# Kernel optimization log

Measured on AMD Instinct MI355X. Metric: run time of the kernel, lower is better.

## Reference

```python
import jax, jax.numpy as jnp
import numpy as np

B, S, D = 8, 2048, 768
H = 4 * D  # MLP hidden
EPS = 1e-5


def setup_inputs() -> dict:
    key = jax.random.key(0)
    ks = jax.random.split(key, 12)
    sd = 1.0 / np.sqrt(D)
    sh = 1.0 / np.sqrt(H)
    return {
        "x": jax.random.normal(ks[0], (B, S, D), dtype=jnp.float32),
        "ln1_g": jnp.ones((D,), jnp.float32),
        "ln1_b": jnp.zeros((D,), jnp.float32),
        "ln2_g": jnp.ones((D,), jnp.float32),
        "ln2_b": jnp.zeros((D,), jnp.float32),
        "Wq": jax.random.normal(ks[1], (D, D), jnp.float32) * sd,
        "bq": jnp.zeros((D,), jnp.float32),
        "Wk": jax.random.normal(ks[2], (D, D), jnp.float32) * sd,
        "bk": jnp.zeros((D,), jnp.float32),
        "Wv": jax.random.normal(ks[3], (D, D), jnp.float32) * sd,
        "bv": jnp.zeros((D,), jnp.float32),
        "Wo": jax.random.normal(ks[4], (D, D), jnp.float32) * sd,
        "bo": jnp.zeros((D,), jnp.float32),
        "Wfc": jax.random.normal(ks[5], (D, H), jnp.float32) * sd,
        "bfc": jnp.zeros((H,), jnp.float32),
        "Wproj": jax.random.normal(ks[6], (H, D), jnp.float32) * sh,
        "bproj": jnp.zeros((D,), jnp.float32),
    }


def _layernorm(x, g, b):
    mu = jnp.mean(x, axis=-1, keepdims=True)
    var = jnp.mean(jnp.square(x - mu), axis=-1, keepdims=True)
    return (x - mu) * jax.lax.rsqrt(var + EPS) * g + b


def reference(x, ln1_g, ln1_b, ln2_g, ln2_b, Wq, bq, Wk, bk, Wv, bv, Wo, bo,
              Wfc, bfc, Wproj, bproj):
    d = x.shape[-1]
    # --- attention sub-block (single head, full D) ---
    h = _layernorm(x, ln1_g, ln1_b)
    q = h @ Wq + bq            # [B,S,D]
    k = h @ Wk + bk
    v = h @ Wv + bv
    scores = jnp.einsum("bsd,btd->bst", q, k) / jnp.sqrt(jnp.float32(d))
    attn = jax.nn.softmax(scores, axis=-1)  # softmax over keys (dim=2)
    y = jnp.einsum("bst,btd->bsd", attn, v)
    x = x + (y @ Wo + bo)
    # --- MLP sub-block (exact GELU like nn.GELU default) ---
    h2 = _layernorm(x, ln2_g, ln2_b)
    m = jax.nn.gelu(h2 @ Wfc + bfc, approximate=False)
    x = x + (m @ Wproj + bproj)  # dropout p=0 -> identity
    return x
```

## Files before the change

kernel.cpp:

```cpp
#include <hip/hip_runtime.h>
#include <hip/hip_bf16.h>

typedef __attribute__((ext_vector_type(8))) short short8;
typedef __attribute__((ext_vector_type(4))) float floatx4;

using bf16 = __hip_bfloat16;

__device__ __forceinline__ void cp16_g2l(bf16* lds_p, const bf16* g) {
  __builtin_amdgcn_global_load_lds(
      (const __attribute__((address_space(1))) unsigned int*)g,
      (__attribute__((address_space(3))) unsigned int*)lds_p,
      16, 0, 0);
}

__device__ __forceinline__ float gelu_exact(float x) {
  return 0.5f * x * (1.0f + erff(x * 0.70710678118654752f));
}

template<int MODE>
__global__ __launch_bounds__(256)
void gemm_bt(const bf16* __restrict__ A, long sAb, long lda,
             const bf16* __restrict__ Bt, long sBb, long ldb,
             const float* __restrict__ bias,
             const float* __restrict__ resid,
             float* __restrict__ rsum, long rsS, long cbStr,
             void* __restrict__ out, long sOb,
             int N, int K, float scale)
{
  constexpr bool PA = (MODE == 5);

  __shared__ __attribute__((aligned(16))) bf16 sA[2][128 * 32];
  __shared__ __attribute__((aligned(16))) bf16 sB[2][128 * 32];

  const int tid = threadIdx.x;
  const int l = tid & 63, w = tid >> 6;
  const int bz = blockIdx.z;
  const long row0 = (long)blockIdx.x * 128;
  const long col0 = (long)blockIdx.y * 128;

  const bf16* Ab = A + (long)bz * sAb;
  const bf16* Bb = Bt + (long)bz * sBb;

  const int sr = (w << 4) + (l >> 2);
  const int slot = (l & 3) ^ ((sr >> 1) & 3);
  const int kcd = (l & 3) << 3;
  const bf16* gA;
  long skipA, koA;
  if constexpr (PA) {
    gA    = Ab + ((long)(slot >> 1) * lda + row0 + sr) * 16 + ((slot & 1) << 3);
    skipA = 64 * 16;
    koA   = 32 * lda;
  } else {
    gA    = Ab + (row0 + sr) * lda + (slot << 3);
    skipA = 64 * lda;
    koA   = 32;
  }
  const bf16* gB = Bb + (col0 + sr) * ldb + (slot << 3);
  const long skipB = 64 * ldb;
  bf16* lA = &sA[0][sr * 32 + kcd];
  bf16* lB = &sB[0][sr * 32 + kcd];

  floatx4 acc[4][4];
  #pragma unroll
  for (int i = 0; i < 4; ++i)
    #pragma unroll
    for (int j = 0; j < 4; ++j)
      acc[i][j] = (floatx4){0.f, 0.f, 0.f, 0.f};

  const int wr = (w >> 1) & 1, wc = w & 1;
  const int g = l >> 4, t = l & 15;
  const int swz = (g ^ ((t >> 1) & 3)) << 3;
  const int aoff = (wr * 64 + t) * 32 + swz;
  const int boff = (wc * 64 + t) * 32 + swz;

  const int nt = K >> 5;

  cp16_g2l(lA,           gA);
  cp16_g2l(lA + 64 * 32, gA + skipA);
  cp16_g2l(lB,           gB);
  cp16_g2l(lB + 64 * 32, gB + skipB);
  __syncthreads();

  for (int kt = 0; kt < nt; ++kt) {
    const int cur = kt & 1;
    if (kt + 1 < nt) {
      const long oA = (long)(kt + 1) * koA;
      const long oB = (long)(kt + 1) << 5;
      bf16* dA = lA + (cur ^ 1) * (128 * 32);
      bf16* dB = lB + (cur ^ 1) * (128 * 32);
      cp16_g2l(dA,           gA + oA);
      cp16_g2l(dA + 64 * 32, gA + oA + skipA);
      cp16_g2l(dB,           gB + oB);
      cp16_g2l(dB + 64 * 32, gB + oB + skipB);
    }
    const bf16* cA = &sA[cur][0];
    const bf16* cB = &sB[cur][0];
    short8 a[4], b[4];
    #pragma unroll
    for (int m = 0; m < 4; ++m) a[m] = *(const short8*)(cA + aoff + m * 512);
    #pragma unroll
    for (int n = 0; n < 4; ++n) b[n] = *(const short8*)(cB + boff + n * 512);
    #pragma unroll
    for (int m = 0; m < 4; ++m)
      #pragma unroll
      for (int n = 0; n < 4; ++n)
        acc[m][n] = __builtin_amdgcn_mfma_f32_16x16x32_bf16(a[m], b[n], acc[m][n], 0, 0, 0);
    __syncthreads();
  }

  const long orow = row0 + wr * 64 + (g << 2);
  const long ocol = col0 + wc * 64 + t;

  if constexpr (MODE == 0 || MODE == 4) {
    bf16* O = (bf16*)out + (long)bz * sOb;
    float bv4[4];
    #pragma unroll
    for (int n = 0; n < 4; ++n) bv4[n] = bias[ocol + n * 16];
    #pragma unroll
    for (int m = 0; m < 4; ++m) {
      #pragma unroll
      for (int r = 0; r < 4; ++r) {
        bf16* Or = O + (orow + m * 16 + r) * (long)N + ocol;
        #pragma unroll
        for (int n = 0; n < 4; ++n) {
          float vv = acc[m][n][r] + bv4[n];
          if constexpr (MODE == 4) vv = gelu_exact(vv);
          Or[n * 16] = __float2bfloat16(vv);
        }
      }
    }
  } else if constexpr (MODE == 3) {
    float* O = (float*)out;
    float bv4[4];
    #pragma unroll
    for (int n = 0; n < 4; ++n) bv4[n] = bias[ocol + n * 16];
    #pragma unroll
    for (int m = 0; m < 4; ++m) {
      #pragma unroll
      for (int r = 0; r < 4; ++r) {
        const long rb = (orow + m * 16 + r) * (long)N + ocol;
        #pragma unroll
        for (int n = 0; n < 4; ++n)
          O[rb + n * 16] = acc[m][n][r] + bv4[n] + resid[rb + n * 16];
      }
    }
  } else if constexpr (MODE == 5) {
    bf16* O = (bf16*)out + (long)bz * sOb;
    #pragma unroll
    for (int m = 0; m < 4; ++m) {
      #pragma unroll
      for (int r = 0; r < 4; ++r) {
        const long rr = orow + m * 16 + r;
        const float inv = 1.0f / rsum[bz * rsS + rr];
        bf16* Or = O + rr * (long)N + ocol;
        #pragma unroll
        for (int n = 0; n < 4; ++n)
          Or[n * 16] = __float2bfloat16(acc[m][n][r] * inv);
      }
    }
  } else {
    bf16* O = (bf16*)out + (long)bz * sOb;
    const long pb = (col0 >> 4) + wc * 4;
    float prow[4][4];
    #pragma unroll
    for (int m = 0; m < 4; ++m)
      #pragma unroll
      for (int r = 0; r < 4; ++r) prow[m][r] = 0.f;
    #pragma unroll
    for (int n = 0; n < 4; ++n) {
      bf16* Opan = O + (pb + n) * (rsS * 16) + t;
      #pragma unroll
      for (int m = 0; m < 4; ++m) {
        #pragma unroll
        for (int r = 0; r < 4; ++r) {
          const float p = __expf(acc[m][n][r] * scale);
          Opan[(orow + m * 16 + r) * 16] = __float2bfloat16(p);
          prow[m][r] += p;
        }
      }
    }
    #pragma unroll
    for (int m = 0; m < 4; ++m) {
      #pragma unroll
      for (int r = 0; r < 4; ++r) {
        float s = prow[m][r];
        s += __shfl_xor(s, 1);
        s += __shfl_xor(s, 2);
        s += __shfl_xor(s, 4);
        s += __shfl_xor(s, 8);
        if (t == 0)
          rsum[(long)(blockIdx.y * 2 + wc) * cbStr + bz * rsS +
               orow + m * 16 + r] = s;
      }
    }
  }
}

__global__ __launch_bounds__(256)
void reduce32(const float* __restrict__ rp, float* __restrict__ rs, int n)
{
  const int i = threadIdx.x + blockIdx.x * 256;
  if (i < n) {
    float s = 0.f;
    #pragma unroll
    for (int c = 0; c < 32; ++c) s += rp[(long)c * 16384 + i];
    rs[i] = s;
  }
}

__global__ __launch_bounds__(256)
void ln_kernel(const float* __restrict__ X, const float* __restrict__ G,
               const float* __restrict__ Bv, bf16* __restrict__ H)
{
  const int tid = threadIdx.x;
  const long row = blockIdx.x;
  const float* xr = X + row * 768;
  const float v0 = xr[tid], v1 = xr[tid + 256], v2 = xr[tid + 512];
  float s = v0 + v1 + v2;
  float s2 = v0 * v0 + v1 * v1 + v2 * v2;
  #pragma unroll
  for (int o = 32; o > 0; o >>= 1) {
    s += __shfl_xor(s, o);
    s2 += __shfl_xor(s2, o);
  }
  __shared__ float red[8];
  const int w = tid >> 6, l = tid & 63;
  if (l == 0) { red[w] = s; red[w + 4] = s2; }
  __syncthreads();
  s = red[0] + red[1] + red[2] + red[3];
  s2 = red[4] + red[5] + red[6] + red[7];
  const float mu = s * (1.f / 768.f);
  const float var = s2 * (1.f / 768.f) - mu * mu;
  const float rstd = rsqrtf(var + 1e-5f);
  bf16* hr = H + row * 768;
  hr[tid]       = __float2bfloat16((v0 - mu) * rstd * G[tid]       + Bv[tid]);
  hr[tid + 256] = __float2bfloat16((v1 - mu) * rstd * G[tid + 256] + Bv[tid + 256]);
  hr[tid + 512] = __float2bfloat16((v2 - mu) * rstd * G[tid + 512] + Bv[tid + 512]);
}

__global__ void transpose_w(const float* __restrict__ W, bf16* __restrict__ Wt,
                            int K, int N)
{
  __shared__ float tile[32][33];
  const int n0 = blockIdx.x * 32, k0 = blockIdx.y * 32;
  const int tx = threadIdx.x, ty = threadIdx.y;
  #pragma unroll
  for (int j = ty; j < 32; j += 8)
    tile[j][tx] = W[(long)(k0 + j) * N + n0 + tx];
  __syncthreads();
  #pragma unroll
  for (int j = ty; j < 32; j += 8)
    Wt[(long)(n0 + j) * K + k0 + tx] = __float2bfloat16(tile[tx][j]);
}

__global__ void transpose_v(const bf16* __restrict__ QKV, bf16* __restrict__ Vt)
{
  __shared__ bf16 tile[32][33];
  const int d0 = blockIdx.x * 32, s0 = blockIdx.y * 32, b = blockIdx.z;
  const int tx = threadIdx.x, ty = threadIdx.y;
  #pragma unroll
  for (int j = ty; j < 32; j += 8)
    tile[j][tx] = QKV[((long)b * 2048 + s0 + j) * 2304 + 1536 + d0 + tx];
  __syncthreads();
  #pragma unroll
  for (int j = ty; j < 32; j += 8)
    Vt[(long)b * 768 * 2048 + (long)(d0 + j) * 2048 + s0 + tx] = tile[tx][j];
}

__global__ void concat3(const float* __restrict__ a, const float* __restrict__ b,
                        const float* __restrict__ c, float* __restrict__ o)
{
  const int i = threadIdx.x + blockIdx.x * 256;
  if (i < 768) { o[i] = a[i]; o[i + 768] = b[i]; o[i + 1536] = c[i]; }
}

extern "C" void kernel_launch(void* const* d_in, const int* in_sizes, int n_in,
                              void* d_out, int out_size, void* d_ws, size_t ws_size,
                              hipStream_t stream)
{
  const float* x     = (const float*)d_in[0];
  const float* ln1g  = (const float*)d_in[1];
  const float* ln1b  = (const float*)d_in[2];
  const float* ln2g  = (const float*)d_in[3];
  const float* ln2b  = (const float*)d_in[4];
  const float* Wq    = (const float*)d_in[5];
  const float* bq    = (const float*)d_in[6];
  const float* Wk    = (const float*)d_in[7];
  const float* bk    = (const float*)d_in[8];
  const float* Wv    = (const float*)d_in[9];
  const float* bvv   = (const float*)d_in[10];
  const float* Wo    = (const float*)d_in[11];
  const float* bo    = (const float*)d_in[12];
  const float* Wfc   = (const float*)d_in[13];
  const float* bfc   = (const float*)d_in[14];
  const float* Wproj = (const float*)d_in[15];
  const float* bproj = (const float*)d_in[16];
  float* out = (float*)d_out;

  constexpr int Bz = 8, S = 2048, D = 768, Hh = 3072, QKVN = 3 * D;
  constexpr long Mtot = (long)Bz * S;

  char* ws = (char*)d_ws;
  size_t off = 0;
  auto alloc = [&](size_t bytes) -> char* {
    char* p = ws + off;
    off += (bytes + 255) & ~(size_t)255;
    return p;
  };
  bf16* wqkvT = (bf16*)alloc((size_t)QKVN * D * 2);
  bf16* woT   = (bf16*)alloc((size_t)D * D * 2);
  bf16* wfcT  = (bf16*)alloc((size_t)Hh * D * 2);
  bf16* wprT  = (bf16*)alloc((size_t)D * Hh * 2);
  float* bqkv = (float*)alloc((size_t)QKVN * 4);
  float* rsum = (float*)alloc((size_t)Mtot * 4);
  float* rpart= (float*)alloc((size_t)32 * Mtot * 4);
  bf16* hb    = (bf16*)alloc((size_t)Mtot * D * 2);
  bf16* qkv   = (bf16*)alloc((size_t)Mtot * QKVN * 2);
  bf16* vtb   = (bf16*)alloc((size_t)Mtot * D * 2);
  bf16* yb    = (bf16*)alloc((size_t)Mtot * D * 2);

  int nbat = Bz;
  size_t region = (size_t)nbat * S * S * 2;
  const size_t mbytes = (size_t)Mtot * Hh * 2;
  if (region < mbytes) region = mbytes;
  if (off + region > ws_size) {
    nbat = 1;
    region = mbytes;
  }
  char* reg = alloc(region);
  bf16* attn = (bf16*)reg;
  bf16* mb = (bf16*)reg;

  const dim3 tb(32, 8);

  transpose_w<<<dim3(D / 32, D / 32), tb, 0, stream>>>(Wq, wqkvT, D, D);
  transpose_w<<<dim3(D / 32, D / 32), tb, 0, stream>>>(Wk, wqkvT + (size_t)D * D, D, D);
  transpose_w<<<dim3(D / 32, D / 32), tb, 0, stream>>>(Wv, wqkvT + 2 * (size_t)D * D, D, D);
  transpose_w<<<dim3(D / 32, D / 32), tb, 0, stream>>>(Wo, woT, D, D);
  transpose_w<<<dim3(Hh / 32, D / 32), tb, 0, stream>>>(Wfc, wfcT, D, Hh);
  transpose_w<<<dim3(D / 32, Hh / 32), tb, 0, stream>>>(Wproj, wprT, Hh, D);
  concat3<<<3, 256, 0, stream>>>(bq, bk, bvv, bqkv);

  ln_kernel<<<(int)Mtot, 256, 0, stream>>>(x, ln1g, ln1b, hb);

  gemm_bt<0><<<dim3(Mtot / 128, QKVN / 128, 1), 256, 0, stream>>>(
      hb, 0, D, wqkvT, 0, D, bqkv, nullptr, nullptr, 0, 0, qkv, 0, QKVN, D, 1.f);
  transpose_v<<<dim3(D / 32, S / 32, Bz), tb, 0, stream>>>(qkv, vtb);

  const float sc = 0.03608439182435161f;
  for (int g0 = 0; g0 < Bz; g0 += nbat) {
    const bf16* qg  = qkv + (long)g0 * S * QKVN;
    const bf16* kg  = qkv + (long)g0 * S * QKVN + D;
    const bf16* vtg = vtb + (long)g0 * D * S;
    float* rsg = rsum + (long)g0 * S;
    float* rpg = rpart + (long)g0 * S;
    bf16* yg = yb + (long)g0 * S * D;
    gemm_bt<6><<<dim3(S / 128, S / 128, nbat), 256, 0, stream>>>(
        qg, (long)S * QKVN, QKVN, kg, (long)S * QKVN, QKVN, nullptr, nullptr,
        rpg, S, Mtot, attn, (long)S * S, S, D, sc);
    reduce32<<<(int)(Mtot / 256), 256, 0, stream>>>(rpart, rsum, (int)Mtot);
    gemm_bt<5><<<dim3(S / 128, D / 128, nbat), 256, 0, stream>>>(
        attn, (long)S * S, S, vtg, (long)D * S, S, nullptr, nullptr,
        rsg, S, 0, yg, (long)S * D, D, S, 1.f);
  }

  gemm_bt<3><<<dim3(Mtot / 128, D / 128, 1), 256, 0, stream>>>(
      yb, 0, D, woT, 0, D, bo, x, nullptr, 0, 0, out, 0, D, D, 1.f);

  ln_kernel<<<(int)Mtot, 256, 0, stream>>>(out, ln2g, ln2b, hb);

  gemm_bt<4><<<dim3(Mtot / 128, Hh / 128, 1), 256, 0, stream>>>(
      hb, 0, D, wfcT, 0, D, bfc, nullptr, nullptr, 0, 0, mb, 0, Hh, D, 1.f);
  gemm_bt<3><<<dim3(Mtot / 128, D / 128, 1), 256, 0, stream>>>(
      mb, 0, Hh, wprT, 0, Hh, bproj, out, nullptr, 0, 0, out, 0, D, Hh, 1.f);
}
```

Measured before the change: 665.0 us.

## Use triple-buffered LDS with one barrier per k-step and partial vmcnt waits

Moves the GEMM main loop from two LDS buffers to three, issues the next tile's global-to-LDS loads, then waits only for the older loads (vmcnt(4)) before a single raw s_barrier. The trailing __syncthreads is removed, because the third buffer keeps the slot being overwritten from matching any slot still being read. The goal is to cut barrier count and let loads overlap MFMA work. In exchange LDS use grows from 32KB to 48KB per block, which may reduce occupancy, and correctness now depends on hand-written waitcnt values.

```diff
diff --git a/kernel.cpp b/kernel.cpp
--- a/kernel.cpp
+++ b/kernel.cpp
@@ -29,8 +29,8 @@
 {
   constexpr bool PA = (MODE == 5);
 
-  __shared__ __attribute__((aligned(16))) bf16 sA[2][128 * 32];
-  __shared__ __attribute__((aligned(16))) bf16 sB[2][128 * 32];
+  __shared__ __attribute__((aligned(16))) bf16 sA[3][128 * 32];
+  __shared__ __attribute__((aligned(16))) bf16 sB[3][128 * 32];
 
   const int tid = threadIdx.x;
   const int l = tid & 63, w = tid >> 6;
@@ -57,8 +57,7 @@
   }
   const bf16* gB = Bb + (col0 + sr) * ldb + (slot << 3);
   const long skipB = 64 * ldb;
-  bf16* lA = &sA[0][sr * 32 + kcd];
-  bf16* lB = &sB[0][sr * 32 + kcd];
+  const int lofs = sr * 32 + kcd;
 
   floatx4 acc[4][4];
   #pragma unroll
@@ -75,26 +74,29 @@
 
   const int nt = K >> 5;
 
-  cp16_g2l(lA,           gA);
-  cp16_g2l(lA + 64 * 32, gA + skipA);
-  cp16_g2l(lB,           gB);
-  cp16_g2l(lB + 64 * 32, gB + skipB);
-  __syncthreads();
-
+  cp16_g2l(&sA[0][lofs],           gA);
+  cp16_g2l(&sA[0][lofs] + 64 * 32, gA + skipA);
+  cp16_g2l(&sB[0][lofs],           gB);
+  cp16_g2l(&sB[0][lofs] + 64 * 32, gB + skipB);
+
+  int bufc = 0;
   for (int kt = 0; kt < nt; ++kt) {
-    const int cur = kt & 1;
+    const int nxtb = (bufc == 2) ? 0 : bufc + 1;
     if (kt + 1 < nt) {
       const long oA = (long)(kt + 1) * koA;
       const long oB = (long)(kt + 1) << 5;
-      bf16* dA = lA + (cur ^ 1) * (128 * 32);
-      bf16* dB = lB + (cur ^ 1) * (128 * 32);
-      cp16_g2l(dA,           gA + oA);
-      cp16_g2l(dA + 64 * 32, gA + oA + skipA);
-      cp16_g2l(dB,           gB + oB);
-      cp16_g2l(dB + 64 * 32, gB + oB + skipB);
-    }
-    const bf16* cA = &sA[cur][0];
-    const bf16* cB = &sB[cur][0];
+      cp16_g2l(&sA[nxtb][lofs],           gA + oA);
+      cp16_g2l(&sA[nxtb][lofs] + 64 * 32, gA + oA + skipA);
+      cp16_g2l(&sB[nxtb][lofs],           gB + oB);
+      cp16_g2l(&sB[nxtb][lofs] + 64 * 32, gB + oB + skipB);
+      asm volatile("s_waitcnt vmcnt(4)" ::: "memory");
+    } else {
+      asm volatile("s_waitcnt vmcnt(0)" ::: "memory");
+    }
+    asm volatile("s_barrier" ::: "memory");
+
+    const bf16* cA = &sA[bufc][0];
+    const bf16* cB = &sB[bufc][0];
     short8 a[4], b[4];
     #pragma unroll
     for (int m = 0; m < 4; ++m) a[m] = *(const short8*)(cA + aoff + m * 512);
@@ -105,7 +107,7 @@
       #pragma unroll
       for (int n = 0; n < 4; ++n)
         acc[m][n] = __builtin_amdgcn_mfma_f32_16x16x32_bf16(a[m], b[n], acc[m][n], 0, 0, 0);
-    __syncthreads();
+    bufc = nxtb;
   }
 
   const long orow = row0 + wr * 64 + (g << 2);
```

Result: faster. 625.6 us (-5.9%).
